# Kernel optimization log

Measured on AMD Instinct MI355X. Metric: run time of the kernel, lower is better.

Reference implementation:

```python
import jax, jax.numpy as jnp
import numpy as np

# Static hyperparams matching init_kwargs
KSIZE, STRIDE, PAD, DIL = 3, 2, 1, 1


def setup_inputs() -> dict:
    key = jax.random.key(0)
    k1, k2 = jax.random.split(key)
    B, H, W, Cin, Cout = 8, 128, 128, 128, 256
    feats = jax.random.normal(k1, (B * H * W, Cin), dtype=jnp.float32)
    weight = jax.random.normal(k2, (KSIZE * KSIZE, Cin, Cout), dtype=jnp.float32) * 0.05
    alpha_upper = jnp.ones((1,), dtype=jnp.float32)
    # dense grid coords [N, 3] = (batch, y, x), matching a dense image sparse tensor
    bb, yy, xx = np.meshgrid(np.arange(B), np.arange(H), np.arange(W), indexing='ij')
    coords = jnp.asarray(np.stack([bb, yy, xx], -1).reshape(-1, 3), dtype=jnp.int32)
    return {"feats": feats, "weight": weight, "alpha_upper": alpha_upper,
            "coords": coords, "H": H, "W": W, "B": B}


def _coord_ranges(H, W):
    # Faithful translation of WrappedMinkowskiStridedOperation.__init__ + forward
    # coordinate math, specialized to a dense grid (per-batch min=0, max=H-1/W-1).
    kernel_origin = DIL * ((KSIZE - 1) // 2) * (KSIZE % 2)
    dilated = DIL * (KSIZE - 1) + 1
    ks_off = kernel_origin - dilated + 1          # _kernel_start_offset
    ke_off = kernel_origin                        # _kernel_end_offset
    idx_start = kernel_origin - PAD               # _index_start_offset
    ranges = []
    for ext in (H, W):
        idx_end = (ext - 1) + kernel_origin + PAD - dilated + 2
        start = max(idx_start, (0 + ks_off - idx_start) // STRIDE * STRIDE + idx_start)
        end = min(idx_end, ((ext - 1 + ke_off - idx_start) // STRIDE + 1) * STRIDE + idx_start)
        ranges.append(np.arange(start, end, STRIDE))
    offsets = np.arange(KSIZE) * DIL - kernel_origin  # kernel region offsets
    return ranges[0], ranges[1], offsets, idx_start


def reference(feats, weight, alpha_upper, coords, H, W, B):
    Cin = feats.shape[1]
    Cout = weight.shape[-1]
    ys, xs, offs, idx_start = _coord_ranges(H, W)
    OH, OW = len(ys), len(xs)
    oy, ox = jnp.meshgrid(jnp.asarray(ys, jnp.int32), jnp.asarray(xs, jnp.int32), indexing='ij')
    dy, dx = np.meshgrid(offs, offs, indexing='ij')
    dy = jnp.asarray(dy.reshape(-1), jnp.int32)  # [kvol]
    dx = jnp.asarray(dx.reshape(-1), jnp.int32)
    ny = oy[None] + dy[:, None, None]            # [kvol, OH, OW]
    nx = ox[None] + dx[:, None, None]
    valid = (ny >= 0) & (ny < H) & (nx >= 0) & (nx < W)
    lin = jnp.clip(ny, 0, H - 1) * W + jnp.clip(nx, 0, W - 1)  # [kvol, OH, OW]
    feats3 = feats.reshape(B, H * W, Cin)
    gathered = feats3[:, lin]                    # [B, kvol, OH, OW, Cin]
    gathered = jnp.where(valid[None, ..., None], gathered, jnp.zeros((), feats.dtype))
    out = jnp.einsum('bkhwc,kcd->bhwd', gathered, weight)  # [B, OH, OW, Cout]
    out_feats = out.reshape(B * OH * OW, Cout)
    # output coordinates, remapped as in forward (shift by index_start, divide by stride)
    oc = jnp.stack([oy, ox], -1).reshape(-1, 2)  # [OH*OW, 2]
    oc = (oc - jnp.int32(idx_start)) // jnp.int32(STRIDE)
    oc = jnp.tile(oc, (B, 1))
    bcol = jnp.repeat(jnp.arange(B, dtype=jnp.int32), OH * OW)
    out_coords = jnp.concatenate([bcol[:, None], oc], axis=1)
    return out_feats, out_coords, alpha_upper
```

## Files before the change

kernel.cpp:

```cpp
#include <hip/hip_runtime.h>


#define OUT_FEATS_ELEMS (32768 * 256)
#define OUT_COORDS_OFF  OUT_FEATS_ELEMS
#define ALPHA_OFF       (OUT_FEATS_ELEMS + 32768 * 3)

typedef float v16f __attribute__((ext_vector_type(16)));

__device__ __forceinline__ unsigned pk4fp8(float a, float b, float c, float d) {
    unsigned u = 0;
    u = __builtin_amdgcn_cvt_pk_fp8_f32(a, b, u, false);
    u = __builtin_amdgcn_cvt_pk_fp8_f32(c, d, u, true);
    return u;
}

#define GLOAD_LDS16(SRC, DST)                                                  \
    __builtin_amdgcn_global_load_lds(                                          \
        (const __attribute__((address_space(1))) void*)(SRC),                  \
        (__attribute__((address_space(3))) void*)(DST), 16, 0, 0)

__global__ void prep_kernel(const float* __restrict__ feats, const float* __restrict__ w,
                            const float* __restrict__ alpha,
                            unsigned char* __restrict__ F8, unsigned char* __restrict__ Bw,
                            float* __restrict__ out) {
    int bid = blockIdx.x;
    if (bid < 8192) {
        int i = bid * 256 + threadIdx.x;
        const float4* f = (const float4*)feats;
        float4 a = f[2 * i];
        float4 b = f[2 * i + 1];
        uint2 r;
        r.x = pk4fp8(a.x, a.y, a.z, a.w);
        r.y = pk4fp8(b.x, b.y, b.z, b.w);
        ((uint2*)F8)[i] = r;
        return;
    }
    int cid = (bid - 8192) * 256 + threadIdx.x;
    if (cid < 32768) {
        int b = cid >> 12, iy = (cid >> 6) & 63, ix = cid & 63;
        float* c = out + OUT_COORDS_OFF + (size_t)cid * 3;
        c[0] = (float)b; c[1] = (float)iy; c[2] = (float)ix;
        if (cid == 0) out[ALPHA_OFF] = alpha[0];
    }
    if (cid < 18432) {
        int ch  = cid & 7;
        int row = (cid >> 3) & 127;
        int t   = cid >> 10;
        int nb  = (t >= 9) ? 1 : 0;
        int tap = t - 9 * nb;
        int chp = ch ^ (row & 7);
        int n   = (nb << 7) + row;
        int kb  = (tap << 7) + (chp << 4);
        unsigned u[4];
#pragma unroll
        for (int q = 0; q < 4; ++q) {
            float f0 = w[(size_t)(kb + 4 * q + 0) * 256 + n];
            float f1 = w[(size_t)(kb + 4 * q + 1) * 256 + n];
            float f2 = w[(size_t)(kb + 4 * q + 2) * 256 + n];
            float f3 = w[(size_t)(kb + 4 * q + 3) * 256 + n];
            u[q] = pk4fp8(f0, f1, f2, f3);
        }
        uint4 r; r.x = u[0]; r.y = u[1]; r.z = u[2]; r.w = u[3];
        *(uint4*)(Bw + (size_t)cid * 16) = r;
    }
}

__global__ void coords_alpha_kernel(float* __restrict__ out, const float* __restrict__ alpha) {
    int i = blockIdx.x * 256 + threadIdx.x;
    int b = i >> 12, iy = (i >> 6) & 63, ix = i & 63;
    float* c = out + OUT_COORDS_OFF + (size_t)i * 3;
    c[0] = (float)b; c[1] = (float)iy; c[2] = (float)ix;
    if (i == 0) out[ALPHA_OFF] = alpha[0];
}

__global__ __launch_bounds__(256, 2) void gemm_conv_kernel(
    const unsigned char* __restrict__ F8,
    const unsigned char* __restrict__ Bw,
    float* __restrict__ out)
{
    __shared__ unsigned char At[2][128 * 128];
    __shared__ unsigned char Bs[2][128 * 128];

    const int tid  = threadIdx.x;
    const int bid  = blockIdx.x;
    const int my   = bid & 255;
    const int nb   = bid >> 8;
    const int n0   = nb << 7;
    const int m0   = my << 7;
    const int bb   = my >> 5;
    const int iy0  = (my << 1) & 63;

    const int lane = tid & 63, wave = tid >> 6;
    const int wm   = (wave >> 1) << 6;
    const int wn   = (wave & 1) << 6;
    const int l31  = lane & 31;
    const int hh   = lane >> 5;
    const int xorl = l31 & 7;

    const int srow = lane >> 3;
    const int chp  = (lane & 7) ^ srow;
    const long rowA0 = (long)bb << 14;
    const unsigned char* bimg = Bw + ((size_t)(nb * 9) << 14) + ((size_t)wave << 12) + ((size_t)lane << 4);

    v16f acc[2][2];
#pragma unroll
    for (int i = 0; i < 2; i++)
#pragma unroll
        for (int j = 0; j < 2; j++) acc[i][j] = (v16f)(0.0f);

    auto stage = [&](int tap, int b) {
        const int dy = tap / 3 - 1;
        const int dx = tap % 3 - 1;
        unsigned char* adst0 = At[b] + (wave << 12);
        unsigned char* bdst0 = Bs[b] + (wave << 12);
#pragma unroll
        for (int it = 0; it < 4; ++it) {
            const int region = (wave << 2) + it;
            GLOAD_LDS16(bimg + ((size_t)tap << 14) + (it << 10), bdst0 + (it << 10));
            const int row = (region << 3) + srow;
            const int iyl = row >> 6, ix = row & 63;
            const int ny  = ((iy0 + iyl) << 1) + dy;
            const int nx  = (ix << 1) + dx;
            if (((unsigned)ny < 128u) & ((unsigned)nx < 128u)) {
                const unsigned char* asrc =
                    F8 + ((rowA0 + ((long)ny << 7) + nx) << 7) + (chp << 4);
                GLOAD_LDS16(asrc, adst0 + (it << 10));
            } else {
                uint4 z; z.x = 0u; z.y = 0u; z.z = 0u; z.w = 0u;
                *(uint4*)(At[b] + (region << 10) + (lane << 4)) = z;
            }
        }
    };

    stage(0, 0);

    for (int tap = 0; tap < 9; ++tap) {
        const int b = tap & 1;
        __syncthreads();
        if (tap < 8) stage(tap + 1, b ^ 1);

#pragma unroll
        for (int seg = 0; seg < 8; ++seg) {
            const int q = seg ^ xorl;
            long long a[2], bb2[2];
#pragma unroll
            for (int i = 0; i < 2; i++)
                a[i] = *(const long long*)(At[b] + ((wm + (i << 5) + l31) << 7) + (q << 4) + (hh << 3));
#pragma unroll
            for (int j = 0; j < 2; j++)
                bb2[j] = *(const long long*)(Bs[b] + ((wn + (j << 5) + l31) << 7) + (q << 4) + (hh << 3));
#pragma unroll
            for (int i = 0; i < 2; i++)
#pragma unroll
                for (int j = 0; j < 2; j++)
                    acc[i][j] = __builtin_amdgcn_mfma_f32_32x32x16_fp8_fp8(a[i], bb2[j], acc[i][j], 0, 0, 0);
        }
    }

#pragma unroll
    for (int i = 0; i < 2; i++)
#pragma unroll
        for (int j = 0; j < 2; j++) {
            const int gcol = n0 + wn + (j << 5) + l31;
#pragma unroll
            for (int r = 0; r < 16; ++r) {
                const int grow = m0 + wm + (i << 5) + (r & 3) + ((r >> 2) << 3) + (hh << 2);
                out[(size_t)grow * 256 + gcol] = acc[i][j][r];
            }
        }
}

__global__ void naive_conv_kernel(const float* __restrict__ feats,
                                  const float* __restrict__ w,
                                  float* __restrict__ out) {
    int m = blockIdx.x;
    int n = threadIdx.x;
    int bb = m >> 12, iy = (m >> 6) & 63, ix = m & 63;
    float acc = 0.f;
    for (int tap = 0; tap < 9; ++tap) {
        int ny = 2 * iy + tap / 3 - 1;
        int nx = 2 * ix + tap % 3 - 1;
        if ((unsigned)ny < 128u && (unsigned)nx < 128u) {
            const float* fr = feats + ((size_t)((bb << 14) + (ny << 7) + nx) << 7);
            const float* wr = w + tap * 32768 + n;
            for (int c = 0; c < 128; ++c) acc += fr[c] * wr[c * 256];
        }
    }
    out[(size_t)m * 256 + n] = acc;
}

extern "C" void kernel_launch(void* const* d_in, const int* in_sizes, int n_in,
                              void* d_out, int out_size, void* d_ws, size_t ws_size,
                              hipStream_t stream) {
    const float* feats  = (const float*)d_in[0];
    const float* weight = (const float*)d_in[1];
    const float* alpha  = (const float*)d_in[2];
    float* out = (float*)d_out;

    const size_t NEED = (size_t)16777216 + (size_t)18 * 16384;
    if (ws_size >= NEED) {
        unsigned char* F8 = (unsigned char*)d_ws;
        unsigned char* Bw = F8 + 16777216;
        prep_kernel<<<8336, 256, 0, stream>>>(feats, weight, alpha, F8, Bw, out);
        gemm_conv_kernel<<<512, 256, 0, stream>>>(F8, Bw, out);
    } else {
        coords_alpha_kernel<<<128, 256, 0, stream>>>(out, alpha);
        naive_conv_kernel<<<32768, 256, 0, stream>>>(feats, weight, out);
    }
}
```

Before: 133.8 us.

## Halve GEMM M-tile to 64 rows, double grid, and map blocks per XCD

The conv GEMM tile shrinks from 128x128 to 64x128 output rows, so each block covers one output image row. This doubles the grid to 1024 blocks, which fills the 256 CUs better, and the launch bound is raised to 3 blocks per CU. Block IDs are remapped so consecutive blocks on the same XCD share output rows and both N halves, which should improve L2 reuse of the A input. In exchange, each wave issues half as many MFMAs per tap, and weights are reloaded per 64 rows, so B traffic per output rises.

```diff
diff --git a/kernel.cpp b/kernel.cpp
--- a/kernel.cpp
+++ b/kernel.cpp
@@ -73,26 +73,28 @@
     if (i == 0) out[ALPHA_OFF] = alpha[0];
 }
 
-__global__ __launch_bounds__(256, 2) void gemm_conv_kernel(
+__global__ __launch_bounds__(256, 3) void gemm_conv_kernel(
     const unsigned char* __restrict__ F8,
     const unsigned char* __restrict__ Bw,
     float* __restrict__ out)
 {
-    __shared__ unsigned char At[2][128 * 128];
+    __shared__ unsigned char At[2][64 * 128];
     __shared__ unsigned char Bs[2][128 * 128];
 
     const int tid  = threadIdx.x;
     const int bid  = blockIdx.x;
-    const int my   = bid & 255;
-    const int nb   = bid >> 8;
+    const int xcd  = bid & 7;
+    const int s    = bid >> 3;
+    const int nb   = s & 1;
+    const int my   = (xcd << 6) + (s >> 1);
     const int n0   = nb << 7;
-    const int m0   = my << 7;
-    const int bb   = my >> 5;
-    const int iy0  = (my << 1) & 63;
+    const int m0   = my << 6;
+    const int bb   = my >> 6;
+    const int iy   = my & 63;
 
     const int lane = tid & 63, wave = tid >> 6;
-    const int wm   = (wave >> 1) << 6;
-    const int wn   = (wave & 1) << 6;
+    const int wm   = (wave & 1) << 5;
+    const int wn   = (wave >> 1) << 6;
     const int l31  = lane & 31;
     const int hh   = lane >> 5;
     const int xorl = l31 & 7;
@@ -102,32 +104,29 @@
     const long rowA0 = (long)bb << 14;
     const unsigned char* bimg = Bw + ((size_t)(nb * 9) << 14) + ((size_t)wave << 12) + ((size_t)lane << 4);
 
-    v16f acc[2][2];
-#pragma unroll
-    for (int i = 0; i < 2; i++)
-#pragma unroll
-        for (int j = 0; j < 2; j++) acc[i][j] = (v16f)(0.0f);
+    v16f acc[2];
+    acc[0] = (v16f)(0.0f); acc[1] = (v16f)(0.0f);
 
     auto stage = [&](int tap, int b) {
         const int dy = tap / 3 - 1;
         const int dx = tap % 3 - 1;
-        unsigned char* adst0 = At[b] + (wave << 12);
-        unsigned char* bdst0 = Bs[b] + (wave << 12);
-#pragma unroll
-        for (int it = 0; it < 4; ++it) {
-            const int region = (wave << 2) + it;
-            GLOAD_LDS16(bimg + ((size_t)tap << 14) + (it << 10), bdst0 + (it << 10));
-            const int row = (region << 3) + srow;
-            const int iyl = row >> 6, ix = row & 63;
-            const int ny  = ((iy0 + iyl) << 1) + dy;
-            const int nx  = (ix << 1) + dx;
-            if (((unsigned)ny < 128u) & ((unsigned)nx < 128u)) {
-                const unsigned char* asrc =
-                    F8 + ((rowA0 + ((long)ny << 7) + nx) << 7) + (chp << 4);
-                GLOAD_LDS16(asrc, adst0 + (it << 10));
+        unsigned char* adst = At[b] + (wave << 11);
+        unsigned char* bdst = Bs[b] + (wave << 12);
+#pragma unroll
+        for (int it = 0; it < 4; ++it)
+            GLOAD_LDS16(bimg + ((size_t)tap << 14) + (it << 10), bdst + (it << 10));
+        const int ny = (iy << 1) + dy;
+        const bool vy = (unsigned)ny < 128u;
+        const long prow = rowA0 + ((long)ny << 7);
+#pragma unroll
+        for (int it = 0; it < 2; ++it) {
+            const int ix = (((wave << 1) + it) << 3) + srow;
+            const int nx = (ix << 1) + dx;
+            if (vy & ((unsigned)nx < 128u)) {
+                GLOAD_LDS16(F8 + ((prow + nx) << 7) + (chp << 4), adst + (it << 10));
             } else {
                 uint4 z; z.x = 0u; z.y = 0u; z.z = 0u; z.w = 0u;
-                *(uint4*)(At[b] + (region << 10) + (lane << 4)) = z;
+                *(uint4*)(At[b] + (((wave << 1) + it) << 10) + (lane << 4)) = z;
             }
         }
     };
@@ -142,32 +141,23 @@
 #pragma unroll
         for (int seg = 0; seg < 8; ++seg) {
             const int q = seg ^ xorl;
-            long long a[2], bb2[2];
-#pragma unroll
-            for (int i = 0; i < 2; i++)
-                a[i] = *(const long long*)(At[b] + ((wm + (i << 5) + l31) << 7) + (q << 4) + (hh << 3));
-#pragma unroll
-            for (int j = 0; j < 2; j++)
-                bb2[j] = *(const long long*)(Bs[b] + ((wn + (j << 5) + l31) << 7) + (q << 4) + (hh << 3));
-#pragma unroll
-            for (int i = 0; i < 2; i++)
-#pragma unroll
-                for (int j = 0; j < 2; j++)
-                    acc[i][j] = __builtin_amdgcn_mfma_f32_32x32x16_fp8_fp8(a[i], bb2[j], acc[i][j], 0, 0, 0);
-        }
-    }
-
-#pragma unroll
-    for (int i = 0; i < 2; i++)
-#pragma unroll
-        for (int j = 0; j < 2; j++) {
-            const int gcol = n0 + wn + (j << 5) + l31;
-#pragma unroll
-            for (int r = 0; r < 16; ++r) {
-                const int grow = m0 + wm + (i << 5) + (r & 3) + ((r >> 2) << 3) + (hh << 2);
-                out[(size_t)grow * 256 + gcol] = acc[i][j][r];
-            }
-        }
+            long long a  = *(const long long*)(At[b] + ((wm + l31) << 7) + (q << 4) + (hh << 3));
+            long long b0 = *(const long long*)(Bs[b] + ((wn + l31) << 7) + (q << 4) + (hh << 3));
+            long long b1 = *(const long long*)(Bs[b] + ((wn + 32 + l31) << 7) + (q << 4) + (hh << 3));
+            acc[0] = __builtin_amdgcn_mfma_f32_32x32x16_fp8_fp8(a, b0, acc[0], 0, 0, 0);
+            acc[1] = __builtin_amdgcn_mfma_f32_32x32x16_fp8_fp8(a, b1, acc[1], 0, 0, 0);
+        }
+    }
+
+#pragma unroll
+    for (int j = 0; j < 2; j++) {
+        const int gcol = n0 + wn + (j << 5) + l31;
+#pragma unroll
+        for (int r = 0; r < 16; ++r) {
+            const int grow = m0 + wm + (r & 3) + ((r >> 2) << 3) + (hh << 2);
+            out[(size_t)grow * 256 + gcol] = acc[j][r];
+        }
+    }
 }
 
 __global__ void naive_conv_kernel(const float* __restrict__ feats,
@@ -202,7 +192,7 @@
         unsigned char* F8 = (unsigned char*)d_ws;
         unsigned char* Bw = F8 + 16777216;
         prep_kernel<<<8336, 256, 0, stream>>>(feats, weight, alpha, F8, Bw, out);
-        gemm_conv_kernel<<<512, 256, 0, stream>>>(F8, Bw, out);
+        gemm_conv_kernel<<<1024, 256, 0, stream>>>(F8, Bw, out);
     } else {
         coords_alpha_kernel<<<128, 256, 0, stream>>>(out, alpha);
         naive_conv_kernel<<<32768, 256, 0, stream>>>(feats, weight, out);
```

Result: slower. 139.1 us (+3.9%).
